# Performance work log

Hardware: AMD Instinct MI355X
Metric: run time of the kernel (lower is better)

## Reference

```python
import jax, jax.numpy as jnp
import numpy as np

D_MODEL = 1024
NUM_HEADS = 16
HEAD_DIM = D_MODEL // NUM_HEADS


def setup_inputs() -> dict:
    key = jax.random.key(0)
    ks = jax.random.split(key, 11)
    B, S = 2, 2048
    sc = 1.0 / np.sqrt(D_MODEL)
    inp = {
        "query": jax.random.normal(ks[0], (B, S, D_MODEL), jnp.float32),
        "key": jax.random.normal(ks[1], (B, S, D_MODEL), jnp.float32),
        "value": jax.random.normal(ks[2], (B, S, D_MODEL), jnp.float32),
        "Wq": jax.random.normal(ks[3], (D_MODEL, D_MODEL), jnp.float32) * sc,
        "bq": jnp.zeros((D_MODEL,), jnp.float32),
        "Wk": jax.random.normal(ks[4], (D_MODEL, D_MODEL), jnp.float32) * sc,
        "bk": jnp.zeros((D_MODEL,), jnp.float32),
        "Wv": jax.random.normal(ks[5], (D_MODEL, D_MODEL), jnp.float32) * sc,
        "bv": jnp.zeros((D_MODEL,), jnp.float32),
        "Wo": jax.random.normal(ks[6], (D_MODEL, D_MODEL), jnp.float32) * sc,
        "bo": jnp.zeros((D_MODEL,), jnp.float32),
    }
    return inp


def _split_heads(x):
    B, S, _ = x.shape
    return x.reshape(B, S, NUM_HEADS, HEAD_DIM).transpose(0, 2, 1, 3)  # [B,H,S,Dh]


def reference(query, key, value, Wq, bq, Wk, bk, Wv, bv, Wo, bo):
    Q = _split_heads(query @ Wq.T + bq)
    K = _split_heads(key @ Wk.T + bk)
    V = _split_heads(value @ Wv.T + bv)
    scores = jnp.einsum("bhqd,bhkd->bhqk", Q, K) / jnp.sqrt(jnp.float32(HEAD_DIM))
    attn = jax.nn.softmax(scores, axis=-1)  # dropout = identity (eval)
    out = jnp.einsum("bhqk,bhkd->bhqd", attn, V)
    B, H, S, Dh = out.shape
    out = out.transpose(0, 2, 1, 3).reshape(B, S, H * Dh)
    return out @ Wo.T + bo
```

## Files before the change

### kernel.cpp

```cpp
#include <hip/hip_runtime.h>
#include <hip/hip_bf16.h>

typedef __attribute__((ext_vector_type(8))) short short8;
typedef __attribute__((ext_vector_type(4))) short short4v;
typedef __attribute__((ext_vector_type(4))) float f32x4;
typedef __attribute__((ext_vector_type(16))) float f32x16;
typedef __attribute__((ext_vector_type(4))) int int4v;
typedef __attribute__((ext_vector_type(2))) int int2v;

#define DEV static __device__ __forceinline__

constexpr int S_LEN   = 2048;
constexpr int DMODEL  = 1024;
constexpr int NHEAD   = 16;
constexpr int DHEAD   = 64;
constexpr int NBATCH  = 2;
constexpr int BHN     = NBATCH * NHEAD;
constexpr int MROWS   = NBATCH * S_LEN;
constexpr int NDIM    = DMODEL;

constexpr float QSCALE = 0.125f * 1.442695041f;

DEV unsigned short f2b(float f) {
  __hip_bfloat16 h = __float2bfloat16(f);
  return __builtin_bit_cast(unsigned short, h);
}
DEV unsigned pk2(float a, float b) {
  return (unsigned)f2b(a) | ((unsigned)f2b(b) << 16);
}
DEV short8 ld8(const void* p) {
  return *reinterpret_cast<const short8*>(p);
}
DEV f32x4 mfma16(short8 a, short8 b, f32x4 c) {
  return __builtin_amdgcn_mfma_f32_16x16x32_bf16(a, b, c, 0, 0, 0);
}
DEV f32x16 mfma32(short8 a, short8 b, f32x16 c) {
  return __builtin_amdgcn_mfma_f32_32x32x16_bf16(a, b, c, 0, 0, 0);
}
DEV void gload16(const void* g, void* l) {
  __builtin_amdgcn_global_load_lds(
      (const __attribute__((address_space(1))) unsigned*)g,
      (__attribute__((address_space(3))) unsigned*)l, 16, 0, 0);
}
DEV float exp2n(float x) {
#if __has_builtin(__builtin_amdgcn_exp2f)
  return __builtin_amdgcn_exp2f(x);
#else
  float r;
  asm("v_exp_f32 %0, %1" : "=v"(r) : "v"(x));
  return r;
#endif
}

struct CvtArgs {
  const float* src[7];
  unsigned short* dst[7];
  int n4[7];
};

__global__ __launch_bounds__(256) void cvt_bf16(CvtArgs c) {
  const int seg = blockIdx.y;
  const float* __restrict__ s = c.src[seg];
  unsigned short* __restrict__ d = c.dst[seg];
  const int n4 = c.n4[seg];
  for (int i = blockIdx.x * 256 + threadIdx.x; i < n4; i += gridDim.x * 256) {
    f32x4 v = reinterpret_cast<const f32x4*>(s)[i];
    short4v r;
    r[0] = (short)f2b(v[0]); r[1] = (short)f2b(v[1]);
    r[2] = (short)f2b(v[2]); r[3] = (short)f2b(v[3]);
    reinterpret_cast<short4v*>(d)[i] = r;
  }
}

struct GB {
  const unsigned short* A[3];
  const unsigned short* W[3];
  const float* bia[3];
  void* out[3];
  int epi[3];
};

DEV void gemm_epilogue(const GB& g, int z, int epi, const float* bia,
                       f32x4 (&acc)[4][2], int bm, int bn, int wr, int wc,
                       int fr, int gq) {
#pragma unroll
  for (int i = 0; i < 4; ++i) {
#pragma unroll
    for (int j = 0; j < 2; ++j) {
#pragma unroll
      for (int r = 0; r < 4; ++r) {
        const int row = bm * 128 + wr * 64 + i * 16 + gq * 4 + r;
        const int col = bn * 64 + wc * 32 + j * 16 + fr;
        float v = acc[i][j][r] + bia[col];
        if (epi == 3) {
          ((float*)g.out[z])[(size_t)row * NDIM + col] = v;
        } else {
          const int b = row >> 11, s = row & (S_LEN - 1);
          const int h = col >> 6,  dh = col & (DHEAD - 1);
          unsigned short* O = (unsigned short*)g.out[z];
          if (epi == 0)      O[((size_t)(b * NHEAD + h) * S_LEN + s) * DHEAD + dh] = f2b(v * QSCALE);
          else if (epi == 1) O[((size_t)(b * NHEAD + h) * S_LEN + s) * DHEAD + dh] = f2b(v);
          else               O[((size_t)(b * NHEAD + h) * DHEAD + dh) * S_LEN + s] = f2b(v);
        }
      }
    }
  }
}

__global__ __launch_bounds__(256, 4) void gemm_k32(GB g) {
  const int cpx = gridDim.x >> 3;
  const int swz = (blockIdx.x & 7) * cpx + (blockIdx.x >> 3);
  const int z   = swz >> 9;
  const int rem = swz & 511;
  const int bm  = rem >> 4, bn = rem & 15;

  const unsigned short* __restrict__ A = g.A[z];
  const unsigned short* __restrict__ W = g.W[z];
  const float* __restrict__ bia = g.bia[z];
  const int epi = g.epi[z];
  const int tid = threadIdx.x, lane = tid & 63, wid = tid >> 6;
  const int wr = wid >> 1, wc = wid & 1;
  const int fr = lane & 15, gq = lane >> 4;

  __shared__ unsigned short As[2][128][32];
  __shared__ unsigned short Bs[2][64][32];

  f32x4 acc[4][2] = {};

  const int srow = lane >> 2;
  const int scol = ((lane & 3) ^ ((srow >> 1) & 3)) * 16;
  const char* aS = (const char*)A + (size_t)(bm * 128 + wid * 32 + srow) * 2048 + scol;
  const char* bS = (const char*)W + (size_t)(bn * 64 + wid * 16 + srow) * 2048 + scol;

  auto stage = [&](int buf, int kt) {
    const int ko = kt * 64;
    char* a0 = (char*)As[buf] + wid * 1024;
    char* b0 = (char*)Bs[buf] + wid * 512;
    gload16(aS + ko, (char*)As[buf] + wid * 2048);
    gload16(aS + (size_t)16 * 2048 + ko, (char*)As[buf] + wid * 2048 + 1024);
    gload16(bS + ko, (char*)Bs[buf] + wid * 1024);
    (void)a0; (void)b0;
  };

  const int rdo = (gq ^ ((fr >> 1) & 3)) * 8;

  stage(0, 0);
  __syncthreads();
  for (int kt = 0; kt < 32; ++kt) {
    const int buf = kt & 1;
    if (kt + 1 < 32) stage(buf ^ 1, kt + 1);
    short8 af[4], bf4[2];
#pragma unroll
    for (int i = 0; i < 4; ++i) af[i] = ld8(&As[buf][wr * 64 + i * 16 + fr][rdo]);
#pragma unroll
    for (int j = 0; j < 2; ++j) bf4[j] = ld8(&Bs[buf][wc * 32 + j * 16 + fr][rdo]);
#pragma unroll
    for (int i = 0; i < 4; ++i)
#pragma unroll
      for (int j = 0; j < 2; ++j)
        acc[i][j] = mfma16(af[i], bf4[j], acc[i][j]);
    __syncthreads();
  }

  gemm_epilogue(g, z, epi, bia, acc, bm, bn, wr, wc, fr, gq);
}

__global__ __launch_bounds__(256, 3) void gemm_k64(GB g) {
  const int cpx = gridDim.x >> 3;
  const int swz = (blockIdx.x & 7) * cpx + (blockIdx.x >> 3);
  const int z   = swz >> 9;
  const int rem = swz & 511;
  const int bm  = rem >> 4, bn = rem & 15;

  const unsigned short* __restrict__ A = g.A[z];
  const unsigned short* __restrict__ W = g.W[z];
  const float* __restrict__ bia = g.bia[z];
  const int epi = g.epi[z];
  const int tid = threadIdx.x, lane = tid & 63, wid = tid >> 6;
  const int wr = wid >> 1, wc = wid & 1;
  const int fr = lane & 15, gq = lane >> 4;

  __shared__ unsigned short As[2][128][64];
  __shared__ unsigned short Bs[2][64][64];

  f32x4 acc[4][2] = {};

  const int srow = lane >> 3;
  const int c8   = lane & 7;
  const int csrc = (c8 ^ (srow & 7)) * 16;
  const char* aS = (const char*)A + (size_t)(bm * 128 + wid * 32 + srow) * 2048 + csrc;
  const char* bS = (const char*)W + (size_t)(bn * 64 + wid * 16 + srow) * 2048 + csrc;

  auto stage = [&](int buf, int kt) {
    const int ko = kt * 128;
    char* a0 = (char*)As[buf] + wid * 4096;
    char* b0 = (char*)Bs[buf] + wid * 2048;
    gload16(aS + ko, a0);
    gload16(aS + (size_t)8 * 2048 + ko, a0 + 1024);
    gload16(aS + (size_t)16 * 2048 + ko, a0 + 2048);
    gload16(aS + (size_t)24 * 2048 + ko, a0 + 3072);
    gload16(bS + ko, b0);
    gload16(bS + (size_t)8 * 2048 + ko, b0 + 1024);
  };

  int rdo[2];
#pragma unroll
  for (int h = 0; h < 2; ++h) rdo[h] = ((4 * h + gq) ^ (fr & 7)) * 8;

  stage(0, 0);
  __syncthreads();
  for (int kt = 0; kt < 16; ++kt) {
    const int buf = kt & 1;
    if (kt + 1 < 16) stage(buf ^ 1, kt + 1);
#pragma unroll
    for (int h = 0; h < 2; ++h) {
      short8 af[4], bf4[2];
#pragma unroll
      for (int i = 0; i < 4; ++i) af[i] = ld8(&As[buf][wr * 64 + i * 16 + fr][rdo[h]]);
#pragma unroll
      for (int j = 0; j < 2; ++j) bf4[j] = ld8(&Bs[buf][wc * 32 + j * 16 + fr][rdo[h]]);
#pragma unroll
      for (int i = 0; i < 4; ++i)
#pragma unroll
        for (int j = 0; j < 2; ++j)
          acc[i][j] = mfma16(af[i], bf4[j], acc[i][j]);
    }
    __syncthreads();
  }

  gemm_epilogue(g, z, epi, bia, acc, bm, bn, wr, wc, fr, gq);
}

__global__ __launch_bounds__(512, 2) void attn_fwd(
    const unsigned short* __restrict__ Qp,
    const unsigned short* __restrict__ Kp,
    const unsigned short* __restrict__ Vt,
    unsigned short* __restrict__ AO) {
  const int nb = (blockIdx.x & 7) * 64 + (blockIdx.x >> 3);
  const int qt = nb & 15, bh = nb >> 4;
  const int tid = threadIdx.x, lane = tid & 63, wid = tid >> 6;
  const int qw = wid & 3, hw = wid >> 2;
  const int ql = lane & 31, hi = lane >> 5, l7 = lane & 7, l3 = lane >> 3;

  const unsigned short* Qh = Qp + (size_t)bh * S_LEN * DHEAD;
  const char* Kh = (const char*)(Kp + (size_t)bh * S_LEN * DHEAD);
  const char* Vh = (const char*)(Vt + (size_t)bh * DHEAD * S_LEN);

  __shared__ unsigned short Klds[2][2][4096];
  __shared__ unsigned short Vlds[2][2][4096];

  const int q0 = qt * 128 + qw * 32;
  short8 qf[4];
#pragma unroll
  for (int d16 = 0; d16 < 4; ++d16)
    qf[d16] = ld8(Qh + (size_t)(q0 + ql) * DHEAD + d16 * 16 + hi * 8);

  const int swc = (l7 ^ l3) << 4;
  const char* kS = Kh + (size_t)hw * 16 * 8192 + (qw * 16 + l3) * 128 + swc;
  const char* vS = Vh + (size_t)hw * 16 * 128 + (qw * 16 + l3) * 4096 + swc;
  char* kD0 = (char*)Klds[hw][0] + qw * 2048;
  char* vD0 = (char*)Vlds[hw][0] + qw * 2048;
  char* kD1 = (char*)Klds[hw][1] + qw * 2048;
  char* vD1 = (char*)Vlds[hw][1] + qw * 2048;

  int xo[4];
#pragma unroll
  for (int j = 0; j < 4; ++j) xo[j] = ((j * 2 + hi) ^ l7) << 4;

  float lacc[8] = {};
  f32x16 o0 = {}, o1 = {};

  gload16(kS, kD0); gload16(kS + 1024, kD0 + 1024);
  gload16(vS, vD0); gload16(vS + 32768, vD0 + 1024);
  __syncthreads();

  constexpr int NT = S_LEN / 64 / 2;
  for (int kt = 0; kt < NT; ++kt) {
    const int buf = kt & 1;
    if (kt + 1 < NT) {
      const char* kn = kS + (kt + 1) * 8192;
      const char* vn = vS + (kt + 1) * 128;
      char* kD = buf ? kD0 : kD1;
      char* vD = buf ? vD0 : vD1;
      gload16(kn, kD); gload16(kn + 1024, kD + 1024);
      gload16(vn, vD); gload16(vn + 32768, vD + 1024);
    }
    const char* kb = (const char*)Klds[hw][buf] + ql * 128;
    const char* vb = (const char*)Vlds[hw][buf] + ql * 128;

    f32x16 st0 = {}, st1 = {};
#pragma unroll
    for (int d16 = 0; d16 < 4; ++d16) {
      short8 k0 = ld8(kb + xo[d16]);
      short8 k1 = ld8(kb + 4096 + xo[d16]);
      st0 = mfma32(k0, qf[d16], st0);
      st1 = mfma32(k1, qf[d16], st1);
    }

#pragma unroll
    for (int r = 0; r < 16; ++r) {
      st0[r] = exp2n(st0[r]);
      st1[r] = exp2n(st1[r]);
    }
#pragma unroll
    for (int r = 0; r < 8; ++r)
      lacc[r] += (st0[r] + st0[r + 8]) + (st1[r] + st1[r + 8]);

#pragma unroll
    for (int ks = 0; ks < 4; ++ks) {
      const f32x16& p = (ks < 2) ? st0 : st1;
      const int a = 8 * (ks & 1);
      unsigned w0 = pk2(p[a + 0], p[a + 1]);
      unsigned w1 = pk2(p[a + 2], p[a + 3]);
      unsigned w2 = pk2(p[a + 4], p[a + 5]);
      unsigned w3 = pk2(p[a + 6], p[a + 7]);
      unsigned x0 = (unsigned)__shfl_xor((int)w0, 32);
      unsigned x1 = (unsigned)__shfl_xor((int)w1, 32);
      unsigned x2 = (unsigned)__shfl_xor((int)w2, 32);
      unsigned x3 = (unsigned)__shfl_xor((int)w3, 32);
      int4v pi;
      pi[0] = (int)(hi ? x2 : w0);
      pi[1] = (int)(hi ? x3 : w1);
      pi[2] = (int)(hi ? w2 : x0);
      pi[3] = (int)(hi ? w3 : x1);
      short8 pb = __builtin_bit_cast(short8, pi);
      short8 v0 = ld8(vb + xo[ks]);
      short8 v1 = ld8(vb + 4096 + xo[ks]);
      o0 = mfma32(v0, pb, o0);
      o1 = mfma32(v1, pb, o1);
    }
    __syncthreads();
  }

#pragma unroll
  for (int s = 4; s; s >>= 1)
#pragma unroll
    for (int r = 0; r < s; ++r) lacc[r] += lacc[r + s];
  float l = lacc[0] + __shfl_xor(lacc[0], 32);

  float* Kf = (float*)&Klds[0][0][0];
  float* Vf = (float*)&Vlds[0][0][0];
  if (hw == 1) {
#pragma unroll
    for (int r = 0; r < 16; ++r) {
      Kf[qw * 2048 + r * 64 + lane]        = o0[r];
      Kf[qw * 2048 + (16 + r) * 64 + lane] = o1[r];
    }
    Vf[qw * 64 + lane] = l;
  }
  __syncthreads();
  if (hw == 0) {
    const float inv = 1.f / (l + Vf[qw * 64 + lane]);
    const int b = bh >> 4, h = bh & 15;
    unsigned short* Op = AO + ((size_t)(b * S_LEN + q0 + ql)) * DMODEL + h * DHEAD;
#pragma unroll
    for (int gidx = 0; gidx < 4; ++gidx) {
      float f0[4], f1[4];
#pragma unroll
      for (int r = 0; r < 4; ++r) {
        const int rr = gidx * 4 + r;
        f0[r] = (o0[rr] + Kf[qw * 2048 + rr * 64 + lane]) * inv;
        f1[r] = (o1[rr] + Kf[qw * 2048 + (16 + rr) * 64 + lane]) * inv;
      }
      int2v s0, s1;
      s0[0] = (int)pk2(f0[0], f0[1]); s0[1] = (int)pk2(f0[2], f0[3]);
      s1[0] = (int)pk2(f1[0], f1[1]); s1[1] = (int)pk2(f1[2], f1[3]);
      *reinterpret_cast<int2v*>(Op + 8 * gidx + 4 * hi)      = s0;
      *reinterpret_cast<int2v*>(Op + 32 + 8 * gidx + 4 * hi) = s1;
    }
  }
}

extern "C" void kernel_launch(void* const* d_in, const int* in_sizes, int n_in,
                              void* d_out, int out_size, void* d_ws, size_t ws_size,
                              hipStream_t stream) {
  const float* query = (const float*)d_in[0];
  const float* key   = (const float*)d_in[1];
  const float* value = (const float*)d_in[2];
  const float* Wq = (const float*)d_in[3];  const float* bq = (const float*)d_in[4];
  const float* Wk = (const float*)d_in[5];  const float* bk = (const float*)d_in[6];
  const float* Wv = (const float*)d_in[7];  const float* bv = (const float*)d_in[8];
  const float* Wo = (const float*)d_in[9];  const float* bo = (const float*)d_in[10];

  const size_t MB = 1024u * 1024u;
  unsigned short* Xb  = (unsigned short*)((char*)d_ws + 0 * MB);
  unsigned short* Wb  = (unsigned short*)((char*)d_ws + 24 * MB);
  unsigned short* Wob = (unsigned short*)((char*)d_ws + 30 * MB);
  unsigned short* Qp  = (unsigned short*)((char*)d_ws + 32 * MB);
  unsigned short* Kp  = (unsigned short*)((char*)d_ws + 40 * MB);
  unsigned short* Vt  = (unsigned short*)((char*)d_ws + 48 * MB);
  unsigned short* AOb = (unsigned short*)((char*)d_ws + 0 * MB);

  const int NACT = MROWS * DMODEL;
  const int NWT  = DMODEL * DMODEL;

  CvtArgs ca;
  ca.src[0] = query; ca.dst[0] = Xb;            ca.n4[0] = NACT / 4;
  ca.src[1] = key;   ca.dst[1] = Xb + NACT;     ca.n4[1] = NACT / 4;
  ca.src[2] = value; ca.dst[2] = Xb + 2 * NACT; ca.n4[2] = NACT / 4;
  ca.src[3] = Wq;    ca.dst[3] = Wb;            ca.n4[3] = NWT / 4;
  ca.src[4] = Wk;    ca.dst[4] = Wb + NWT;      ca.n4[4] = NWT / 4;
  ca.src[5] = Wv;    ca.dst[5] = Wb + 2 * NWT;  ca.n4[5] = NWT / 4;
  ca.src[6] = Wo;    ca.dst[6] = Wob;           ca.n4[6] = NWT / 4;
  cvt_bf16<<<dim3(512, 7), 256, 0, stream>>>(ca);

  GB g1;
  g1.A[0] = Xb;            g1.A[1] = Xb + NACT; g1.A[2] = Xb + 2 * NACT;
  g1.W[0] = Wb;            g1.W[1] = Wb + NWT;  g1.W[2] = Wb + 2 * NWT;
  g1.bia[0] = bq;  g1.bia[1] = bk; g1.bia[2] = bv;
  g1.out[0] = Qp;  g1.out[1] = Kp; g1.out[2] = Vt;
  g1.epi[0] = 0;   g1.epi[1] = 1;  g1.epi[2] = 2;
  gemm_k32<<<dim3(16 * 32 * 3), 256, 0, stream>>>(g1);

  attn_fwd<<<dim3(BHN * 16), 512, 0, stream>>>(Qp, Kp, Vt, AOb);

  GB g2 = {};
  g2.A[0] = AOb; g2.W[0] = Wob; g2.bia[0] = bo; g2.out[0] = d_out; g2.epi[0] = 3;
  gemm_k64<<<dim3(16 * 32), 256, 0, stream>>>(g2);
}
```

Before: 148.9 us.

## Split attention key range four ways per block and read V directly from global

The attention kernel now processes 64 query rows per block instead of 128 and splits the key sequence across four wave pairs, doubling the grid. V is no longer staged in LDS; each wave loads its V fragments directly from global memory, and only K stays double-buffered in shared memory. The partial outputs and row sums from the four splits are combined through LDS in two passes. This trades higher grid parallelism and lower LDS use for uncoalesced global V loads and a heavier reduction epilogue.

```diff
diff --git a/kernel.cpp b/kernel.cpp
--- a/kernel.cpp
+++ b/kernel.cpp
@@ -134,12 +134,9 @@
 
   auto stage = [&](int buf, int kt) {
     const int ko = kt * 64;
-    char* a0 = (char*)As[buf] + wid * 1024;
-    char* b0 = (char*)Bs[buf] + wid * 512;
     gload16(aS + ko, (char*)As[buf] + wid * 2048);
     gload16(aS + (size_t)16 * 2048 + ko, (char*)As[buf] + wid * 2048 + 1024);
     gload16(bS + ko, (char*)Bs[buf] + wid * 1024);
-    (void)a0; (void)b0;
   };
 
   const int rdo = (gq ^ ((fr >> 1) & 3)) * 8;
@@ -236,84 +233,69 @@
     const unsigned short* __restrict__ Kp,
     const unsigned short* __restrict__ Vt,
     unsigned short* __restrict__ AO) {
-  const int nb = (blockIdx.x & 7) * 64 + (blockIdx.x >> 3);
-  const int qt = nb & 15, bh = nb >> 4;
+  const int nb = (blockIdx.x & 7) * 128 + (blockIdx.x >> 3);
+  const int qt = nb & 31, bh = nb >> 5;
   const int tid = threadIdx.x, lane = tid & 63, wid = tid >> 6;
-  const int qw = wid & 3, hw = wid >> 2;
+  const int qw2 = wid & 1, hw4 = wid >> 1;
   const int ql = lane & 31, hi = lane >> 5, l7 = lane & 7, l3 = lane >> 3;
 
   const unsigned short* Qh = Qp + (size_t)bh * S_LEN * DHEAD;
   const char* Kh = (const char*)(Kp + (size_t)bh * S_LEN * DHEAD);
   const char* Vh = (const char*)(Vt + (size_t)bh * DHEAD * S_LEN);
 
-  __shared__ unsigned short Klds[2][2][4096];
-  __shared__ unsigned short Vlds[2][2][4096];
-
-  const int q0 = qt * 128 + qw * 32;
+  __shared__ unsigned short Klds[4][2][2048];
+
+  const int q0 = qt * 64 + qw2 * 32;
   short8 qf[4];
 #pragma unroll
   for (int d16 = 0; d16 < 4; ++d16)
     qf[d16] = ld8(Qh + (size_t)(q0 + ql) * DHEAD + d16 * 16 + hi * 8);
 
   const int swc = (l7 ^ l3) << 4;
-  const char* kS = Kh + (size_t)hw * 16 * 8192 + (qw * 16 + l3) * 128 + swc;
-  const char* vS = Vh + (size_t)hw * 16 * 128 + (qw * 16 + l3) * 4096 + swc;
-  char* kD0 = (char*)Klds[hw][0] + qw * 2048;
-  char* vD0 = (char*)Vlds[hw][0] + qw * 2048;
-  char* kD1 = (char*)Klds[hw][1] + qw * 2048;
-  char* vD1 = (char*)Vlds[hw][1] + qw * 2048;
+  const char* kS = Kh + (size_t)hw4 * 512 * 128 + (qw2 * 16 + l3) * 128 + swc;
+  char* kD0 = (char*)Klds[hw4][0] + qw2 * 2048;
+  char* kD1 = (char*)Klds[hw4][1] + qw2 * 2048;
 
   int xo[4];
 #pragma unroll
   for (int j = 0; j < 4; ++j) xo[j] = ((j * 2 + hi) ^ l7) << 4;
+
+  const char* vG0 = Vh + (size_t)ql * 4096 + hw4 * 1024;
+  const char* vG1 = vG0 + (size_t)32 * 4096;
 
   float lacc[8] = {};
   f32x16 o0 = {}, o1 = {};
 
   gload16(kS, kD0); gload16(kS + 1024, kD0 + 1024);
-  gload16(vS, vD0); gload16(vS + 32768, vD0 + 1024);
-  __syncthreads();
-
-  constexpr int NT = S_LEN / 64 / 2;
+  __syncthreads();
+
+  constexpr int NT = 512 / 32;
   for (int kt = 0; kt < NT; ++kt) {
     const int buf = kt & 1;
     if (kt + 1 < NT) {
-      const char* kn = kS + (kt + 1) * 8192;
-      const char* vn = vS + (kt + 1) * 128;
+      const char* kn = kS + (kt + 1) * 4096;
       char* kD = buf ? kD0 : kD1;
-      char* vD = buf ? vD0 : vD1;
       gload16(kn, kD); gload16(kn + 1024, kD + 1024);
-      gload16(vn, vD); gload16(vn + 32768, vD + 1024);
-    }
-    const char* kb = (const char*)Klds[hw][buf] + ql * 128;
-    const char* vb = (const char*)Vlds[hw][buf] + ql * 128;
-
-    f32x16 st0 = {}, st1 = {};
-#pragma unroll
-    for (int d16 = 0; d16 < 4; ++d16) {
-      short8 k0 = ld8(kb + xo[d16]);
-      short8 k1 = ld8(kb + 4096 + xo[d16]);
-      st0 = mfma32(k0, qf[d16], st0);
-      st1 = mfma32(k1, qf[d16], st1);
-    }
-
-#pragma unroll
-    for (int r = 0; r < 16; ++r) {
-      st0[r] = exp2n(st0[r]);
-      st1[r] = exp2n(st1[r]);
-    }
-#pragma unroll
-    for (int r = 0; r < 8; ++r)
-      lacc[r] += (st0[r] + st0[r + 8]) + (st1[r] + st1[r + 8]);
-
-#pragma unroll
-    for (int ks = 0; ks < 4; ++ks) {
-      const f32x16& p = (ks < 2) ? st0 : st1;
-      const int a = 8 * (ks & 1);
-      unsigned w0 = pk2(p[a + 0], p[a + 1]);
-      unsigned w1 = pk2(p[a + 2], p[a + 3]);
-      unsigned w2 = pk2(p[a + 4], p[a + 5]);
-      unsigned w3 = pk2(p[a + 6], p[a + 7]);
+    }
+    const char* kb = (const char*)Klds[hw4][buf] + ql * 128;
+
+    f32x16 st = {};
+#pragma unroll
+    for (int d16 = 0; d16 < 4; ++d16)
+      st = mfma32(ld8(kb + xo[d16]), qf[d16], st);
+
+#pragma unroll
+    for (int r = 0; r < 16; ++r) st[r] = exp2n(st[r]);
+#pragma unroll
+    for (int r = 0; r < 8; ++r) lacc[r] += st[r] + st[r + 8];
+
+#pragma unroll
+    for (int ks = 0; ks < 2; ++ks) {
+      const int a = ks * 8;
+      unsigned w0 = pk2(st[a + 0], st[a + 1]);
+      unsigned w1 = pk2(st[a + 2], st[a + 3]);
+      unsigned w2 = pk2(st[a + 4], st[a + 5]);
+      unsigned w3 = pk2(st[a + 6], st[a + 7]);
       unsigned x0 = (unsigned)__shfl_xor((int)w0, 32);
       unsigned x1 = (unsigned)__shfl_xor((int)w1, 32);
       unsigned x2 = (unsigned)__shfl_xor((int)w2, 32);
@@ -324,8 +306,8 @@
       pi[2] = (int)(hi ? w2 : x0);
       pi[3] = (int)(hi ? w3 : x1);
       short8 pb = __builtin_bit_cast(short8, pi);
-      short8 v0 = ld8(vb + xo[ks]);
-      short8 v1 = ld8(vb + 4096 + xo[ks]);
+      short8 v0 = ld8(vG0 + kt * 64 + (ks * 2 + hi) * 16);
+      short8 v1 = ld8(vG1 + kt * 64 + (ks * 2 + hi) * 16);
       o0 = mfma32(v0, pb, o0);
       o1 = mfma32(v1, pb, o1);
     }
@@ -339,33 +321,57 @@
   float l = lacc[0] + __shfl_xor(lacc[0], 32);
 
   float* Kf = (float*)&Klds[0][0][0];
-  float* Vf = (float*)&Vlds[0][0][0];
-  if (hw == 1) {
-#pragma unroll
-    for (int r = 0; r < 16; ++r) {
-      Kf[qw * 2048 + r * 64 + lane]        = o0[r];
-      Kf[qw * 2048 + (16 + r) * 64 + lane] = o1[r];
-    }
-    Vf[qw * 64 + lane] = l;
-  }
-  __syncthreads();
-  if (hw == 0) {
-    const float inv = 1.f / (l + Vf[qw * 64 + lane]);
-    const int b = bh >> 4, h = bh & 15;
-    unsigned short* Op = AO + ((size_t)(b * S_LEN + q0 + ql)) * DMODEL + h * DHEAD;
+  float* Lf = Kf + 6144;
+  __syncthreads();
+  if (hw4) {
+#pragma unroll
+    for (int r = 0; r < 16; ++r)
+      Kf[((hw4 - 1) * 2 + qw2) * 1024 + r * 64 + lane] = o0[r];
+    Lf[(hw4 - 1) * 128 + qw2 * 64 + lane] = l;
+  }
+  __syncthreads();
+  float inv = 0.f;
+  const int b = bh >> 4, h = bh & 15;
+  unsigned short* Op = AO + ((size_t)(b * S_LEN + q0 + ql)) * DMODEL + h * DHEAD;
+  if (hw4 == 0) {
+    const float lt = l + Lf[qw2 * 64 + lane] + Lf[128 + qw2 * 64 + lane]
+                       + Lf[256 + qw2 * 64 + lane];
+    inv = 1.f / lt;
 #pragma unroll
     for (int gidx = 0; gidx < 4; ++gidx) {
-      float f0[4], f1[4];
+      float f0[4];
 #pragma unroll
       for (int r = 0; r < 4; ++r) {
         const int rr = gidx * 4 + r;
-        f0[r] = (o0[rr] + Kf[qw * 2048 + rr * 64 + lane]) * inv;
-        f1[r] = (o1[rr] + Kf[qw * 2048 + (16 + rr) * 64 + lane]) * inv;
+        f0[r] = (o0[rr] + Kf[(qw2)*1024 + rr * 64 + lane]
+                        + Kf[(2 + qw2) * 1024 + rr * 64 + lane]
+                        + Kf[(4 + qw2) * 1024 + rr * 64 + lane]) * inv;
       }
-      int2v s0, s1;
+      int2v s0;
       s0[0] = (int)pk2(f0[0], f0[1]); s0[1] = (int)pk2(f0[2], f0[3]);
+      *reinterpret_cast<int2v*>(Op + 8 * gidx + 4 * hi) = s0;
+    }
+  }
+  __syncthreads();
+  if (hw4) {
+#pragma unroll
+    for (int r = 0; r < 16; ++r)
+      Kf[((hw4 - 1) * 2 + qw2) * 1024 + r * 64 + lane] = o1[r];
+  }
+  __syncthreads();
+  if (hw4 == 0) {
+#pragma unroll
+    for (int gidx = 0; gidx < 4; ++gidx) {
+      float f1[4];
+#pragma unroll
+      for (int r = 0; r < 4; ++r) {
+        const int rr = gidx * 4 + r;
+        f1[r] = (o1[rr] + Kf[(qw2)*1024 + rr * 64 + lane]
+                        + Kf[(2 + qw2) * 1024 + rr * 64 + lane]
+                        + Kf[(4 + qw2) * 1024 + rr * 64 + lane]) * inv;
+      }
+      int2v s1;
       s1[0] = (int)pk2(f1[0], f1[1]); s1[1] = (int)pk2(f1[2], f1[3]);
-      *reinterpret_cast<int2v*>(Op + 8 * gidx + 4 * hi)      = s0;
       *reinterpret_cast<int2v*>(Op + 32 + 8 * gidx + 4 * hi) = s1;
     }
   }
@@ -412,7 +418,7 @@
   g1.epi[0] = 0;   g1.epi[1] = 1;  g1.epi[2] = 2;
   gemm_k32<<<dim3(16 * 32 * 3), 256, 0, stream>>>(g1);
 
-  attn_fwd<<<dim3(BHN * 16), 512, 0, stream>>>(Qp, Kp, Vt, AOb);
+  attn_fwd<<<dim3(BHN * 32), 512, 0, stream>>>(Qp, Kp, Vt, AOb);
 
   GB g2 = {};
   g2.A[0] = AOb; g2.W[0] = Wob; g2.bia[0] = bo; g2.out[0] = d_out; g2.epi[0] = 3;
```

Measured after the change: 174.6 us. 1.17x slower.
